# Performance work log

Hardware: AMD Instinct MI355X
Metric: run time of the kernel (lower is better)

The kernel has to match this reference:

```python
import jax, jax.numpy as jnp
import numpy as np

N_NODES = 100_000
N_EDGES = 3_200_000
D_IN = 128
D_OUT = 128


def setup_inputs() -> dict:
    key = jax.random.key(0)
    k1, k2, k3, k4 = jax.random.split(key, 4)
    x = jax.random.normal(k1, (N_NODES, D_IN), dtype=jnp.float32)
    edge_index = jax.random.randint(k2, (2, N_EDGES), 0, N_NODES, dtype=jnp.int32)
    # nn.Linear(in, out): W is [out, in], b is [out]
    W = jax.random.normal(k3, (D_OUT, D_IN), dtype=jnp.float32) * (1.0 / np.sqrt(D_IN))
    b = jax.random.normal(k4, (D_OUT,), dtype=jnp.float32) * 0.01
    return {"x": x, "edge_index": edge_index, "W": W, "b": b}


def reference(x, edge_index, W, b):
    row, col = edge_index[0], edge_index[1]
    # deg = bincount(row); symmetric-normalization coefficients per edge
    deg = jax.ops.segment_sum(jnp.ones(row.shape[0], dtype=x.dtype), row,
                              num_segments=N_NODES)
    deg_inv_sqrt = jnp.where(deg > 0, jax.lax.rsqrt(deg), 0.0)
    norm = deg_inv_sqrt[row] * deg_inv_sqrt[col]  # [E]
    # linear transform then SpMM aggregation: out[i] = sum_{e: row[e]=i} norm[e] * xl[col[e]]
    xl = x @ W.T + b  # [N, D_OUT]
    out = jax.ops.segment_sum(norm[:, None] * xl[col], row, num_segments=N_NODES)
    return out
```

## Files before the change

### kernel.cpp

```cpp
#include <hip/hip_runtime.h>
#include <hip/hip_bf16.h>

#define N_NODES 100000
#define N_EDGES 3200000
#define D 128
#define NB 782
#define CAP 5120
#define EPB 16

typedef __attribute__((ext_vector_type(8))) short short8v;
typedef __attribute__((ext_vector_type(4))) float f32x4;

static __device__ __forceinline__ short f2bf(float f) {
    __hip_bfloat16 h = __float2bfloat16(f);
    return __builtin_bit_cast(short, h);
}

__global__ __launch_bounds__(256) void init_cursor(int* __restrict__ cursor) {
    int i = blockIdx.x * 256 + threadIdx.x;
    if (i < NB) cursor[i] = i * CAP;
}

__global__ __launch_bounds__(256) void partition_k(const int* __restrict__ ei,
                                                   int* __restrict__ cursor,
                                                   int* __restrict__ staging) {
    __shared__ int lbin[NB];
    __shared__ int lcnt[NB];
    int tid = threadIdx.x;
    long long base = (long long)blockIdx.x * (256 * EPB);

    for (int i = tid; i < NB; i += 256) lbin[i] = 0;
    __syncthreads();

    int lrank[EPB];
#pragma unroll
    for (int j = 0; j < EPB; ++j) {
        long long e = base + j * 256 + tid;
        lrank[j] = -1;
        if (e < N_EDGES) {
            int r = ei[e];
            lrank[j] = atomicAdd(&lbin[r >> 7], 1);
        }
    }
    __syncthreads();
    for (int i = tid; i < NB; i += 256) {
        int c = lbin[i];
        lcnt[i] = c;
        if (c > 0) lbin[i] = atomicAdd(&cursor[i], c);
    }
    __syncthreads();
#pragma unroll
    for (int j = 0; j < EPB; ++j) {
        long long e = base + j * 256 + tid;
        if (e < N_EDGES) {
            int r = ei[e];
            int c = ei[N_EDGES + e];
            int bin = r >> 7;
            staging[lbin[bin] + lrank[j]] = (c << 7) | (r & 127);
        }
    }
    (void)lcnt;
}

__global__ __launch_bounds__(1024) void bscan_k(const int* __restrict__ cursor,
                                                int* __restrict__ fbase) {
    __shared__ int s[1024];
    int tid = threadIdx.x;
    int v = (tid < NB) ? (cursor[tid] - tid * CAP) : 0;
    s[tid] = v;
    __syncthreads();
    for (int off = 1; off < 1024; off <<= 1) {
        int t = (tid >= off) ? s[tid - off] : 0;
        __syncthreads();
        s[tid] += t;
        __syncthreads();
    }
    if (tid < NB) fbase[tid] = s[tid] - v;
    if (tid == NB - 1) fbase[NB] = s[tid];
}

__global__ __launch_bounds__(256) void pass2_k(const int* __restrict__ staging,
                                               const int* __restrict__ cursor,
                                               const int* __restrict__ fbase,
                                               int* __restrict__ rowptr,
                                               float* __restrict__ dinv,
                                               int* __restrict__ edgesF) {
    __shared__ int hist[128];
    __shared__ int ssc[128];
    __shared__ int lrk[128];
    int bin = blockIdx.x;
    int tid = threadIdx.x;
    int cnt = cursor[bin] - bin * CAP;
    int fb = fbase[bin];
    int row0 = bin << 7;
    const int* st = staging + bin * CAP;

    if (tid < 128) { hist[tid] = 0; lrk[tid] = 0; }
    __syncthreads();
    for (int i = tid; i < cnt; i += 256)
        atomicAdd(&hist[st[i] & 127], 1);
    __syncthreads();
    if (tid < 128) ssc[tid] = hist[tid];
    __syncthreads();
    for (int off = 1; off < 128; off <<= 1) {
        int t = (tid < 128 && tid >= off) ? ssc[tid - off] : 0;
        __syncthreads();
        if (tid < 128) ssc[tid] += t;
        __syncthreads();
    }
    if (tid < 128) {
        int row = row0 + tid;
        if (row < N_NODES) {
            int deg = hist[tid];
            rowptr[row] = fb + ssc[tid] - deg;
            dinv[row] = (deg > 0) ? rsqrtf((float)deg) : 0.0f;
        }
    }
    if (bin == 0 && tid == 0) rowptr[N_NODES] = N_EDGES;
    __syncthreads();
    for (int i = tid; i < cnt; i += 256) {
        int rec = st[i];
        int r = rec & 127;
        int c = ((unsigned)rec) >> 7;
        int k = atomicAdd(&lrk[r], 1);
        edgesF[fb + ssc[r] - hist[r] + k] = c;
    }
}

__global__ __launch_bounds__(256) void convW(const float* __restrict__ W,
                                             __hip_bfloat16* __restrict__ Wb) {
    int i = blockIdx.x * 256 + threadIdx.x;
    if (i < D * D) Wb[i] = __float2bfloat16(W[i]);
}

__global__ __launch_bounds__(256) void gemm_mfma(const float* __restrict__ x,
                                                 const __hip_bfloat16* __restrict__ Wb,
                                                 const float* __restrict__ b,
                                                 __hip_bfloat16* __restrict__ xl) {
    __shared__ __hip_bfloat16 lds[4][16][136];
    int tid = threadIdx.x;
    int w = tid >> 6;
    int l = tid & 63;
    int lm = l & 15;
    int kb = l >> 4;
    int bm = blockIdx.x * 64 + w * 16;

    int row = bm + lm;
    if (row >= N_NODES) row = N_NODES - 1;
    const float* xr = x + (size_t)row * D;

    short8v a[4];
#pragma unroll
    for (int ks = 0; ks < 4; ++ks) {
        const float* p = xr + ks * 32 + kb * 8;
        float4 u = *(const float4*)p;
        float4 v = *(const float4*)(p + 4);
        short8v t;
        t[0] = f2bf(u.x); t[1] = f2bf(u.y); t[2] = f2bf(u.z); t[3] = f2bf(u.w);
        t[4] = f2bf(v.x); t[5] = f2bf(v.y); t[6] = f2bf(v.z); t[7] = f2bf(v.w);
        a[ks] = t;
    }

    f32x4 acc[8];
#pragma unroll
    for (int nf = 0; nf < 8; ++nf) {
        acc[nf][0] = 0.f; acc[nf][1] = 0.f; acc[nf][2] = 0.f; acc[nf][3] = 0.f;
    }

    const short8v* Wv = reinterpret_cast<const short8v*>(Wb);
#pragma unroll
    for (int ks = 0; ks < 4; ++ks) {
#pragma unroll
        for (int nf = 0; nf < 8; ++nf) {
            short8v bf = Wv[(nf * 16 + lm) * 16 + ks * 4 + kb];
            acc[nf] = __builtin_amdgcn_mfma_f32_16x16x32_bf16(a[ks], bf, acc[nf], 0, 0, 0);
        }
    }

#pragma unroll
    for (int nf = 0; nf < 8; ++nf) {
        float bias = b[nf * 16 + lm];
#pragma unroll
        for (int j = 0; j < 4; ++j) {
            lds[w][kb * 4 + j][nf * 16 + lm] = __float2bfloat16(acc[nf][j] + bias);
        }
    }
    __syncthreads();
#pragma unroll
    for (int it = 0; it < 4; ++it) {
        int idx = it * 64 + l;
        int r = idx >> 4;
        int ch = (idx & 15) * 8;
        int grow = bm + r;
        if (grow < N_NODES)
            *(short8v*)&xl[(size_t)grow * D + ch] = *(const short8v*)&lds[w][r][ch];
    }
}

__global__ __launch_bounds__(256) void aggregate(const int* __restrict__ edges,
                                                 const int* __restrict__ rowptr,
                                                 const float* __restrict__ dinv,
                                                 const unsigned int* __restrict__ xl2,
                                                 float* __restrict__ out) {
    int gw = (blockIdx.x * 256 + threadIdx.x) >> 6;
    int lane = threadIdx.x & 63;
    if (gw >= N_NODES) return;
    int s = rowptr[gw];
    int e = rowptr[gw + 1];
    float dr = dinv[gw];
    float ax = 0.0f, ay = 0.0f;
    int i = s;
    for (; i + 4 <= e; i += 4) {
        int c0 = edges[i], c1 = edges[i + 1], c2 = edges[i + 2], c3 = edges[i + 3];
        float w0 = dr * dinv[c0], w1 = dr * dinv[c1];
        float w2 = dr * dinv[c2], w3 = dr * dinv[c3];
        unsigned int v0 = xl2[c0 * 64 + lane];
        unsigned int v1 = xl2[c1 * 64 + lane];
        unsigned int v2 = xl2[c2 * 64 + lane];
        unsigned int v3 = xl2[c3 * 64 + lane];
        ax += w0 * __uint_as_float(v0 << 16);
        ay += w0 * __uint_as_float(v0 & 0xffff0000u);
        ax += w1 * __uint_as_float(v1 << 16);
        ay += w1 * __uint_as_float(v1 & 0xffff0000u);
        ax += w2 * __uint_as_float(v2 << 16);
        ay += w2 * __uint_as_float(v2 & 0xffff0000u);
        ax += w3 * __uint_as_float(v3 << 16);
        ay += w3 * __uint_as_float(v3 & 0xffff0000u);
    }
    for (; i < e; ++i) {
        int c0 = edges[i];
        float w0 = dr * dinv[c0];
        unsigned int v0 = xl2[c0 * 64 + lane];
        ax += w0 * __uint_as_float(v0 << 16);
        ay += w0 * __uint_as_float(v0 & 0xffff0000u);
    }
    float2 r;
    r.x = ax;
    r.y = ay;
    *(float2*)&out[(size_t)gw * D + lane * 2] = r;
}

extern "C" void kernel_launch(void* const* d_in, const int* in_sizes, int n_in,
                              void* d_out, int out_size, void* d_ws, size_t ws_size,
                              hipStream_t stream) {
    const float* x  = (const float*)d_in[0];
    const int*   ei = (const int*)d_in[1];
    const float* W  = (const float*)d_in[2];
    const float* b  = (const float*)d_in[3];
    float* out = (float*)d_out;

    unsigned int* ws = (unsigned int*)d_ws;
    __hip_bfloat16* xl = (__hip_bfloat16*)ws;
    __hip_bfloat16* Wb = (__hip_bfloat16*)(ws + 6400000);
    float* dinv    = (float*)(ws + 6408192);
    int*   rowptr  = (int*)(ws + 6508288);
    int*   cursor  = (int*)(ws + 6608448);
    int*   fbase   = (int*)(ws + 6609248);
    int*   edgesF  = (int*)(ws + 6610048);
    int*   staging = (int*)(ws + 9810048);

    init_cursor<<<(NB + 255) / 256, 256, 0, stream>>>(cursor);

    const int pblocks = (N_EDGES + 256 * EPB - 1) / (256 * EPB);
    partition_k<<<pblocks, 256, 0, stream>>>(ei, cursor, staging);

    bscan_k<<<1, 1024, 0, stream>>>(cursor, fbase);

    convW<<<(D * D + 255) / 256, 256, 0, stream>>>(W, Wb);

    pass2_k<<<NB, 256, 0, stream>>>(staging, cursor, fbase, rowptr, dinv, edgesF);

    gemm_mfma<<<(N_NODES + 63) / 64, 256, 0, stream>>>(x, Wb, b, xl);

    aggregate<<<(N_NODES * 64 + 255) / 256, 256, 0, stream>>>(
        edgesF, rowptr, dinv, (const unsigned int*)xl, out);
}
```

Measured before the change: 352.3 us.

## Fold column degree scaling into GEMM epilogue and cache edge records in registers

The GEMM epilogue now scales each transformed row by its dinv value, so the aggregation no longer gathers dinv[col] per edge and applies the row normalization once at the end. The partition kernel keeps packed records and ranks in registers instead of reloading edge_index. The CSR pass keeps staged records and their ranks in registers, which removes the second staging read and the second atomic pass. The GEMM now depends on dinv, so pass2 is moved before it, and the bf16 rounding now happens after the scaling.

After: 319.7 us. 1.1x faster.

```diff
diff --git a/kernel.cpp b/kernel.cpp
--- a/kernel.cpp
+++ b/kernel.cpp
@@ -7,6 +7,7 @@
 #define NB 782
 #define CAP 5120
 #define EPB 16
+#define K2 20
 
 typedef __attribute__((ext_vector_type(8))) short short8v;
 typedef __attribute__((ext_vector_type(4))) float f32x4;
@@ -25,41 +26,41 @@
                                                    int* __restrict__ cursor,
                                                    int* __restrict__ staging) {
     __shared__ int lbin[NB];
-    __shared__ int lcnt[NB];
     int tid = threadIdx.x;
     long long base = (long long)blockIdx.x * (256 * EPB);
 
     for (int i = tid; i < NB; i += 256) lbin[i] = 0;
     __syncthreads();
 
-    int lrank[EPB];
+    int lrec[EPB];
+    int lpk[EPB];
 #pragma unroll
     for (int j = 0; j < EPB; ++j) {
         long long e = base + j * 256 + tid;
-        lrank[j] = -1;
-        if (e < N_EDGES) {
-            int r = ei[e];
-            lrank[j] = atomicAdd(&lbin[r >> 7], 1);
-        }
-    }
-    __syncthreads();
-    for (int i = tid; i < NB; i += 256) {
-        int c = lbin[i];
-        lcnt[i] = c;
-        if (c > 0) lbin[i] = atomicAdd(&cursor[i], c);
-    }
-    __syncthreads();
-#pragma unroll
-    for (int j = 0; j < EPB; ++j) {
-        long long e = base + j * 256 + tid;
+        lpk[j] = -1;
         if (e < N_EDGES) {
             int r = ei[e];
             int c = ei[N_EDGES + e];
             int bin = r >> 7;
-            staging[lbin[bin] + lrank[j]] = (c << 7) | (r & 127);
-        }
-    }
-    (void)lcnt;
+            int rank = atomicAdd(&lbin[bin], 1);
+            lrec[j] = (c << 7) | (r & 127);
+            lpk[j] = (bin << 16) | rank;
+        }
+    }
+    __syncthreads();
+    for (int i = tid; i < NB; i += 256) {
+        int c = lbin[i];
+        if (c > 0) lbin[i] = atomicAdd(&cursor[i], c);
+    }
+    __syncthreads();
+#pragma unroll
+    for (int j = 0; j < EPB; ++j) {
+        if (lpk[j] >= 0) {
+            int bin = ((unsigned)lpk[j]) >> 16;
+            int rank = lpk[j] & 0xffff;
+            staging[lbin[bin] + rank] = lrec[j];
+        }
+    }
 }
 
 __global__ __launch_bounds__(1024) void bscan_k(const int* __restrict__ cursor,
@@ -76,7 +77,6 @@
         __syncthreads();
     }
     if (tid < NB) fbase[tid] = s[tid] - v;
-    if (tid == NB - 1) fbase[NB] = s[tid];
 }
 
 __global__ __launch_bounds__(256) void pass2_k(const int* __restrict__ staging,
@@ -87,7 +87,6 @@
                                                int* __restrict__ edgesF) {
     __shared__ int hist[128];
     __shared__ int ssc[128];
-    __shared__ int lrk[128];
     int bin = blockIdx.x;
     int tid = threadIdx.x;
     int cnt = cursor[bin] - bin * CAP;
@@ -95,10 +94,20 @@
     int row0 = bin << 7;
     const int* st = staging + bin * CAP;
 
-    if (tid < 128) { hist[tid] = 0; lrk[tid] = 0; }
-    __syncthreads();
-    for (int i = tid; i < cnt; i += 256)
-        atomicAdd(&hist[st[i] & 127], 1);
+    if (tid < 128) hist[tid] = 0;
+    __syncthreads();
+
+    int myrec[K2];
+    int myrank[K2];
+#pragma unroll
+    for (int k = 0; k < K2; ++k) {
+        int idx = k * 256 + tid;
+        myrec[k] = (idx < cnt) ? st[idx] : -1;
+    }
+#pragma unroll
+    for (int k = 0; k < K2; ++k) {
+        myrank[k] = (myrec[k] >= 0) ? atomicAdd(&hist[myrec[k] & 127], 1) : 0;
+    }
     __syncthreads();
     if (tid < 128) ssc[tid] = hist[tid];
     __syncthreads();
@@ -118,12 +127,13 @@
     }
     if (bin == 0 && tid == 0) rowptr[N_NODES] = N_EDGES;
     __syncthreads();
-    for (int i = tid; i < cnt; i += 256) {
-        int rec = st[i];
-        int r = rec & 127;
-        int c = ((unsigned)rec) >> 7;
-        int k = atomicAdd(&lrk[r], 1);
-        edgesF[fb + ssc[r] - hist[r] + k] = c;
+#pragma unroll
+    for (int k = 0; k < K2; ++k) {
+        if (myrec[k] >= 0) {
+            int r = myrec[k] & 127;
+            int c = ((unsigned)myrec[k]) >> 7;
+            edgesF[fb + ssc[r] - hist[r] + myrank[k]] = c;
+        }
     }
 }
 
@@ -136,6 +146,7 @@
 __global__ __launch_bounds__(256) void gemm_mfma(const float* __restrict__ x,
                                                  const __hip_bfloat16* __restrict__ Wb,
                                                  const float* __restrict__ b,
+                                                 const float* __restrict__ dinv,
                                                  __hip_bfloat16* __restrict__ xl) {
     __shared__ __hip_bfloat16 lds[4][16][136];
     int tid = threadIdx.x;
@@ -177,12 +188,21 @@
         }
     }
 
+    float drj[4];
+#pragma unroll
+    for (int j = 0; j < 4; ++j) {
+        int rr = bm + kb * 4 + j;
+        if (rr >= N_NODES) rr = N_NODES - 1;
+        drj[j] = dinv[rr];
+    }
+
 #pragma unroll
     for (int nf = 0; nf < 8; ++nf) {
         float bias = b[nf * 16 + lm];
 #pragma unroll
         for (int j = 0; j < 4; ++j) {
-            lds[w][kb * 4 + j][nf * 16 + lm] = __float2bfloat16(acc[nf][j] + bias);
+            lds[w][kb * 4 + j][nf * 16 + lm] =
+                __float2bfloat16((acc[nf][j] + bias) * drj[j]);
         }
     }
     __syncthreads();
@@ -207,36 +227,32 @@
     if (gw >= N_NODES) return;
     int s = rowptr[gw];
     int e = rowptr[gw + 1];
-    float dr = dinv[gw];
     float ax = 0.0f, ay = 0.0f;
     int i = s;
     for (; i + 4 <= e; i += 4) {
         int c0 = edges[i], c1 = edges[i + 1], c2 = edges[i + 2], c3 = edges[i + 3];
-        float w0 = dr * dinv[c0], w1 = dr * dinv[c1];
-        float w2 = dr * dinv[c2], w3 = dr * dinv[c3];
         unsigned int v0 = xl2[c0 * 64 + lane];
         unsigned int v1 = xl2[c1 * 64 + lane];
         unsigned int v2 = xl2[c2 * 64 + lane];
         unsigned int v3 = xl2[c3 * 64 + lane];
-        ax += w0 * __uint_as_float(v0 << 16);
-        ay += w0 * __uint_as_float(v0 & 0xffff0000u);
-        ax += w1 * __uint_as_float(v1 << 16);
-        ay += w1 * __uint_as_float(v1 & 0xffff0000u);
-        ax += w2 * __uint_as_float(v2 << 16);
-        ay += w2 * __uint_as_float(v2 & 0xffff0000u);
-        ax += w3 * __uint_as_float(v3 << 16);
-        ay += w3 * __uint_as_float(v3 & 0xffff0000u);
+        ax += __uint_as_float(v0 << 16);
+        ay += __uint_as_float(v0 & 0xffff0000u);
+        ax += __uint_as_float(v1 << 16);
+        ay += __uint_as_float(v1 & 0xffff0000u);
+        ax += __uint_as_float(v2 << 16);
+        ay += __uint_as_float(v2 & 0xffff0000u);
+        ax += __uint_as_float(v3 << 16);
+        ay += __uint_as_float(v3 & 0xffff0000u);
     }
     for (; i < e; ++i) {
-        int c0 = edges[i];
-        float w0 = dr * dinv[c0];
-        unsigned int v0 = xl2[c0 * 64 + lane];
-        ax += w0 * __uint_as_float(v0 << 16);
-        ay += w0 * __uint_as_float(v0 & 0xffff0000u);
-    }
+        unsigned int v0 = xl2[edges[i] * 64 + lane];
+        ax += __uint_as_float(v0 << 16);
+        ay += __uint_as_float(v0 & 0xffff0000u);
+    }
+    float dr = dinv[gw];
     float2 r;
-    r.x = ax;
-    r.y = ay;
+    r.x = dr * ax;
+    r.y = dr * ay;
     *(float2*)&out[(size_t)gw * D + lane * 2] = r;
 }
 
@@ -266,11 +282,11 @@
 
     bscan_k<<<1, 1024, 0, stream>>>(cursor, fbase);
 
+    pass2_k<<<NB, 256, 0, stream>>>(staging, cursor, fbase, rowptr, dinv, edgesF);
+
     convW<<<(D * D + 255) / 256, 256, 0, stream>>>(W, Wb);
 
-    pass2_k<<<NB, 256, 0, stream>>>(staging, cursor, fbase, rowptr, dinv, edgesF);
-
-    gemm_mfma<<<(N_NODES + 63) / 64, 256, 0, stream>>>(x, Wb, b, xl);
+    gemm_mfma<<<(N_NODES + 63) / 64, 256, 0, stream>>>(x, Wb, b, dinv, xl);
 
     aggregate<<<(N_NODES * 64 + 255) / 256, 256, 0, stream>>>(
         edgesF, rowptr, dinv, (const unsigned int*)xl, out);
```
